# Kernel optimization log

Hardware: AMD Instinct MI355X
Metric: run time of the kernel (lower is better)

Reference implementation:

```python
import jax, jax.numpy as jnp
import numpy as np

N, E, D, ED, H, MAXDEG = 50000, 800000, 128, 64, 8, 512
C = D // H


def _ln(x, g, b, eps=1e-5):
    m = jnp.mean(x, axis=-1, keepdims=True)
    v = jnp.var(x, axis=-1, keepdims=True)
    return (x - m) * jax.lax.rsqrt(v + eps) * g + b


def setup_inputs() -> dict:
    key = jax.random.key(0)
    ks = jax.random.split(key, 16)
    nrm = lambda k, s: jax.random.normal(k, s, jnp.float32) * 0.02
    return {
        "x": jax.random.normal(ks[0], (N, D), jnp.float32),
        "edge_index": jax.random.randint(ks[1], (2, E), 0, N, dtype=jnp.int32),
        "edge_attr": jax.random.normal(ks[2], (E, ED), jnp.float32),
        "deg_emb": nrm(ks[3], (MAXDEG, D)),
        "ln_g": jnp.ones((D,), jnp.float32), "ln_b": jnp.zeros((D,), jnp.float32),
        "Wq": nrm(ks[4], (D, D)), "bq": jnp.zeros((D,), jnp.float32),
        "Wk": nrm(ks[5], (D, D)), "bk": jnp.zeros((D,), jnp.float32),
        "Wv": nrm(ks[6], (D, D)), "bv": jnp.zeros((D,), jnp.float32),
        "We": nrm(ks[7], (ED, D)), "be": jnp.zeros((D,), jnp.float32),
        "Wskip": nrm(ks[8], (D, D)), "bskip": jnp.zeros((D,), jnp.float32),
        "W1": nrm(ks[9], (D, 4 * D)), "b1": jnp.zeros((4 * D,), jnp.float32),
        "W2": nrm(ks[10], (4 * D, D)), "b2": jnp.zeros((D,), jnp.float32),
        "eu_ln_g": jnp.ones((D,), jnp.float32), "eu_ln_b": jnp.zeros((D,), jnp.float32),
        "Wm": nrm(ks[11], (2 * D + ED, 2 * ED)), "bm": jnp.zeros((2 * ED,), jnp.float32),
        "eln_g": jnp.ones((ED,), jnp.float32), "eln_b": jnp.zeros((ED,), jnp.float32),
    }


def reference(x, edge_index, edge_attr, deg_emb, ln_g, ln_b, Wq, bq, Wk, bk, Wv, bv,
              We, be, Wskip, bskip, W1, b1, W2, b2, eu_ln_g, eu_ln_b, Wm, bm, eln_g, eln_b):
    n = x.shape[0]
    src, dst = edge_index[0], edge_index[1]

    # degree embedding: out-degree via scatter-add on src, clamped
    deg = jax.ops.segment_sum(jnp.ones_like(src), src, num_segments=n)
    x_in = x + deg_emb[jnp.clip(deg, 0, MAXDEG - 1)]

    # pre-norm (same LayerNorm module used for attn and ffn branches)
    h = _ln(x_in, ln_g, ln_b)

    # TransformerConv: per-edge gather -> score -> segment softmax -> scatter
    q = (h @ Wq + bq).reshape(n, H, C)
    k = (h @ Wk + bk).reshape(n, H, C)
    v = (h @ Wv + bv).reshape(n, H, C)
    e = (edge_attr @ We + be).reshape(-1, H, C)  # [E,H,C]

    ke = k[src] + e
    alpha = jnp.sum(q[dst] * ke, axis=-1) / jnp.sqrt(jnp.float32(C))  # [E,H]
    amax = jax.ops.segment_max(alpha, dst, num_segments=n)
    amax = jnp.where(jnp.isfinite(amax), amax, 0.0)
    ex = jnp.exp(alpha - amax[dst])
    denom = jax.ops.segment_sum(ex, dst, num_segments=n)
    w = ex / (denom[dst] + 1e-16)  # [E,H]

    msg = (v[src] + e) * w[:, :, None]
    out = jax.ops.segment_sum(msg, dst, num_segments=n).reshape(n, D)
    h_attn = out + h @ Wskip + bskip  # root skip on normed input

    x_attn = x_in + h_attn

    # FFN with pre-norm (norm_type == 'layer')
    hf = _ln(x_attn, ln_g, ln_b)
    ffn = jax.nn.gelu(hf @ W1 + b1, approximate=False) @ W2 + b2
    x_new = x_attn + ffn

    # EdgeUpdate: gated residual MLP on gathered node pairs
    xn = _ln(x_new, eu_ln_g, eu_ln_b)
    m = jnp.concatenate([xn[src], xn[dst], edge_attr], axis=-1)  # [E, 2D+ED]
    raw = jax.nn.relu(m @ Wm + bm)
    delta, gate = jnp.split(raw, 2, axis=-1)
    ea_new = _ln(edge_attr + jax.nn.sigmoid(gate) * delta, eln_g, eln_b)

    return x_new, ea_new
```

## Files before the change

kernel.cpp:

```cpp
#include <hip/hip_runtime.h>
#include <hip/hip_bf16.h>
#include <math.h>

constexpr int N_NODES = 50000;
constexpr int N_EDGES = 800000;
constexpr int D  = 128;
constexpr int ED = 64;

typedef __attribute__((ext_vector_type(8))) short short8;
typedef __attribute__((ext_vector_type(4))) float f32x4;

static __device__ __forceinline__ float allsum64(float v){
#pragma unroll
  for(int off=32; off>=1; off>>=1) v += __shfl_xor(v, off, 64);
  return v;
}

static __device__ __forceinline__ short bfs(float f){
  __hip_bfloat16 h = __float2bfloat16(f);
  return *reinterpret_cast<short*>(&h);
}
static __device__ __forceinline__ float bf2f(short s){
  __hip_bfloat16 h = *reinterpret_cast<__hip_bfloat16*>(&s);
  return __bfloat162float(h);
}

template<typename T> __device__ __forceinline__ T cvt_out(float v);
template<> __device__ __forceinline__ float cvt_out<float>(float v){ return v; }
template<> __device__ __forceinline__ __hip_bfloat16 cvt_out<__hip_bfloat16>(float v){ return __float2bfloat16(v); }

__global__ void k_deg(const int* __restrict__ src, const int* __restrict__ dst,
                      int* __restrict__ deg, int* __restrict__ hist){
  int i = blockIdx.x*256 + threadIdx.x;
  if(i < N_EDGES){
    atomicAdd(&deg[src[i]], 1);
    atomicAdd(&hist[dst[i]], 1);
  }
}

__global__ __launch_bounds__(1024) void k_scan(const int* __restrict__ hist,
                                               int* __restrict__ rows,
                                               int* __restrict__ cursor){
  __shared__ int part[1024];
  const int t = threadIdx.x;
  const int CH = (N_NODES + 1023) / 1024;
  int base = t*CH;
  int s = 0;
  for(int i=0;i<CH;i++){ int idx=base+i; if(idx<N_NODES) s += hist[idx]; }
  part[t] = s; __syncthreads();
  for(int off=1; off<1024; off<<=1){
    int v = (t>=off) ? part[t-off] : 0;
    __syncthreads();
    part[t] += v;
    __syncthreads();
  }
  int run = part[t] - s;
  for(int i=0;i<CH;i++){
    int idx=base+i;
    if(idx<N_NODES){ rows[idx]=run; cursor[idx]=run; run += hist[idx]; }
  }
  if(t==1023) rows[N_NODES] = run;
}

__global__ void k_scatter(const int* __restrict__ src, const int* __restrict__ dst,
                          int* __restrict__ cursor,
                          int* __restrict__ perm, int* __restrict__ ssrc){
  int e = blockIdx.x*256 + threadIdx.x;
  if(e < N_EDGES){
    int p = atomicAdd(&cursor[dst[e]], 1);
    perm[p] = e;
    ssrc[p] = src[e];
  }
}

__global__ __launch_bounds__(256) void k_node_prep(
    const float* __restrict__ x, const int* __restrict__ deg,
    const float* __restrict__ deg_emb, const float* __restrict__ g,
    const float* __restrict__ b, float* __restrict__ xin, float* __restrict__ h){
  int node = blockIdx.x*4 + (threadIdx.x>>6);
  int lane = threadIdx.x & 63;
  if(node >= N_NODES) return;
  int dg = deg[node]; dg = dg > 511 ? 511 : dg;
  const float* xr = x + (size_t)node*D;
  const float* er = deg_emb + (size_t)dg*D;
  float a0 = xr[lane]    + er[lane];
  float a1 = xr[lane+64] + er[lane+64];
  float* xo = xin + (size_t)node*D;
  xo[lane] = a0; xo[lane+64] = a1;
  float s  = allsum64(a0+a1);
  float s2 = allsum64(a0*a0 + a1*a1);
  float mean = s * (1.f/128.f);
  float var  = s2 * (1.f/128.f) - mean*mean;
  float rs = rsqrtf(var + 1e-5f);
  float* ho = h + (size_t)node*D;
  ho[lane]    = (a0-mean)*rs*g[lane]    + b[lane];
  ho[lane+64] = (a1-mean)*rs*g[lane+64] + b[lane+64];
}

__global__ void k_pack(const float* __restrict__ Wq, const float* __restrict__ Wk,
                       const float* __restrict__ Wv, const float* __restrict__ Ws,
                       const float* __restrict__ bq, const float* __restrict__ bk,
                       const float* __restrict__ bv, const float* __restrict__ bs,
                       float* __restrict__ Wcat, float* __restrict__ bcat){
  int idx = blockIdx.x*256 + threadIdx.x;
  if(idx < D*4*D){
    int i = idx >> 9, j = idx & 511;
    int sel = j >> 7, jj = j & 127;
    const float* W = sel==0?Wq: sel==1?Wk: sel==2?Wv:Ws;
    Wcat[idx] = W[i*D + jj];
  } else if(idx < D*4*D + 4*D){
    int j = idx - D*4*D;
    int sel = j>>7, jj = j&127;
    const float* B = sel==0?bq: sel==1?bk: sel==2?bv:bs;
    bcat[j] = B[jj];
  }
}

__global__ void k_packWN(const float* __restrict__ W, short* __restrict__ out,
                         int K, int Nfull){
  int idx = blockIdx.x*256 + threadIdx.x;
  if(idx >= K*Nfull) return;
  int KC = K >> 5;
  int j  = idx & 7;
  int l  = (idx>>3) & 63;
  int cf = (idx>>9) & 7;
  int rest = idx >> 12;
  int kc = rest % KC;
  int nb = rest / KC;
  int k = kc*32 + ((l>>4)<<3) + j;
  int n = nb*128 + (cf<<4) + (l&15);
  out[idx] = bfs(W[(size_t)k*Nfull + n]);
}

template<int ACT, bool SRCADD, typename OutT, typename AT>
__global__ __launch_bounds__(256) void k_gemm_mfma(
    const AT* __restrict__ A, const short* __restrict__ Wp,
    const float* __restrict__ bias, const float* __restrict__ Src,
    OutT* __restrict__ C, int M, int K, int Nfull){
  const int tid = threadIdx.x, lane = tid & 63, wid = tid >> 6;
  const int l16 = lane & 15, lg = lane >> 4;
  const int KC = K >> 5;
  const size_t rowb = (size_t)blockIdx.x*64 + wid*16;
  const int nb = blockIdx.y;
  size_t arow = rowb + l16; if(arow >= (size_t)M) arow = M-1;
  f32x4 acc[8] = {};
  const short8* Bg = ((const short8*)Wp) + (size_t)nb*KC*512 + lane;
  for(int kc=0; kc<KC; kc++){
    short8 a;
    if constexpr (sizeof(AT)==4){
      const float* ap = (const float*)A + arow*K + kc*32 + lg*8;
      float4 f0 = *(const float4*)ap;
      float4 f1 = *(const float4*)(ap+4);
      a[0]=bfs(f0.x); a[1]=bfs(f0.y); a[2]=bfs(f0.z); a[3]=bfs(f0.w);
      a[4]=bfs(f1.x); a[5]=bfs(f1.y); a[6]=bfs(f1.z); a[7]=bfs(f1.w);
    } else {
      a = *(const short8*)((const short*)A + arow*K + kc*32 + lg*8);
    }
#pragma unroll
    for(int cf=0;cf<8;cf++){
      short8 b = Bg[(kc*8+cf)*64];
      acc[cf] = __builtin_amdgcn_mfma_f32_16x16x32_bf16(a, b, acc[cf], 0, 0, 0);
    }
  }
#pragma unroll
  for(int cf=0;cf<8;cf++){
    int col = nb*128 + cf*16 + l16;
    float bb = bias[col];
#pragma unroll
    for(int r=0;r<4;r++){
      size_t ro = rowb + lg*4 + r;
      if(ro < (size_t)M){
        float v = acc[cf][r] + bb;
        if(ACT == 1) v = v * 0.5f * (1.f + erff(v * 0.70710678118f));
        if(SRCADD) v += Src[ro*Nfull + col];
        C[ro*Nfull + col] = cvt_out<OutT>(v);
      }
    }
  }
}

__global__ __launch_bounds__(256) void k_eproj_sorted(
    const float* __restrict__ eattr, const int* __restrict__ perm,
    const short* __restrict__ Wep, const float* __restrict__ be,
    __hip_bfloat16* __restrict__ out){
  const int tid = threadIdx.x, lane = tid & 63, wid = tid >> 6;
  const int l16 = lane & 15, lg = lane >> 4;
  const size_t row = (size_t)blockIdx.x*64 + wid*16;
  const int pe = perm[row + l16];
  f32x4 acc[8] = {};
  const short8* Bg = ((const short8*)Wep) + lane;
  const float* ga = eattr + (size_t)pe*64;
#pragma unroll
  for(int kc=0;kc<2;kc++){
    int cb = kc*32 + lg*8;
    float4 f0 = *(const float4*)(ga + cb);
    float4 f1 = *(const float4*)(ga + cb + 4);
    short8 a;
    a[0]=bfs(f0.x); a[1]=bfs(f0.y); a[2]=bfs(f0.z); a[3]=bfs(f0.w);
    a[4]=bfs(f1.x); a[5]=bfs(f1.y); a[6]=bfs(f1.z); a[7]=bfs(f1.w);
#pragma unroll
    for(int cf=0;cf<8;cf++){
      short8 b = Bg[(kc*8+cf)*64];
      acc[cf] = __builtin_amdgcn_mfma_f32_16x16x32_bf16(a, b, acc[cf], 0, 0, 0);
    }
  }
#pragma unroll
  for(int cf=0;cf<8;cf++){
    int col = cf*16 + l16;
    float bb = be[col];
#pragma unroll
    for(int r=0;r<4;r++){
      size_t ro = row + lg*4 + r;
      out[ro*128 + col] = __float2bfloat16(acc[cf][r] + bb);
    }
  }
}

__global__ __launch_bounds__(256) void k_attn_fused2(
    const int* __restrict__ ssrc, const int* __restrict__ rows,
    const short* __restrict__ qk, const short* __restrict__ es,
    const float* __restrict__ xin, const float* __restrict__ g,
    const float* __restrict__ b,
    float* __restrict__ xattn, float* __restrict__ hf){
  int n = blockIdx.x*4 + (threadIdx.x>>6);
  int lane = threadIdx.x & 63;
  if(n >= N_NODES) return;
  const short* qrow = qk + (size_t)n*512;
  float q0 = bf2f(qrow[lane]), q1 = bf2f(qrow[lane+64]);
  float m0=-INFINITY, m1=-INFINITY;
  float den0=0.f, den1=0.f, acc0=0.f, acc1=0.f;
  int i = rows[n];
  const int i1 = rows[n+1];

  auto body = [&](float eA0, float eA1, float kv0, float kv1, float kv2, float kv3){
    float p0 = q0*(kv0 + eA0);
    float p1 = q1*(kv1 + eA1);
    p0 += __shfl_xor(p0,1,64); p0 += __shfl_xor(p0,2,64);
    p0 += __shfl_xor(p0,4,64); p0 += __shfl_xor(p0,8,64);
    p1 += __shfl_xor(p1,1,64); p1 += __shfl_xor(p1,2,64);
    p1 += __shfl_xor(p1,4,64); p1 += __shfl_xor(p1,8,64);
    float a0 = p0*0.25f, a1 = p1*0.25f;
    float v0 = kv2 + eA0, v1 = kv3 + eA1;
    float mn0 = fmaxf(m0,a0), mn1 = fmaxf(m1,a1);
    float sc0 = __expf(m0-mn0), sc1 = __expf(m1-mn1);
    float ex0 = __expf(a0-mn0), ex1 = __expf(a1-mn1);
    den0 = den0*sc0 + ex0;       den1 = den1*sc1 + ex1;
    acc0 = acc0*sc0 + ex0*v0;    acc1 = acc1*sc1 + ex1*v1;
    m0 = mn0; m1 = mn1;
  };

  for(; i+2 <= i1; i += 2){
    int sA = ssrc[i], sB = ssrc[i+1];
    const short* eA = es + (size_t)i*128;
    const short* kA = qk + (size_t)sA*512 + 128;
    const short* kB = qk + (size_t)sB*512 + 128;
    float eA0=bf2f(eA[lane]),      eA1=bf2f(eA[lane+64]);
    float eB0=bf2f(eA[lane+128]),  eB1=bf2f(eA[lane+192]);
    float kA0=bf2f(kA[lane]),      kA1=bf2f(kA[lane+64]);
    float vA0=bf2f(kA[lane+128]),  vA1=bf2f(kA[lane+192]);
    float kB0=bf2f(kB[lane]),      kB1=bf2f(kB[lane+64]);
    float vB0=bf2f(kB[lane+128]),  vB1=bf2f(kB[lane+192]);
    float pA0 = q0*(kA0+eA0), pA1 = q1*(kA1+eA1);
    float pB0 = q0*(kB0+eB0), pB1 = q1*(kB1+eB1);
#pragma unroll
    for(int off=1; off<16; off<<=1){
      pA0 += __shfl_xor(pA0,off,64); pA1 += __shfl_xor(pA1,off,64);
      pB0 += __shfl_xor(pB0,off,64); pB1 += __shfl_xor(pB1,off,64);
    }
    {
      float a0 = pA0*0.25f, a1 = pA1*0.25f;
      float v0 = vA0+eA0, v1 = vA1+eA1;
      float mn0 = fmaxf(m0,a0), mn1 = fmaxf(m1,a1);
      float sc0 = __expf(m0-mn0), sc1 = __expf(m1-mn1);
      float ex0 = __expf(a0-mn0), ex1 = __expf(a1-mn1);
      den0 = den0*sc0 + ex0;       den1 = den1*sc1 + ex1;
      acc0 = acc0*sc0 + ex0*v0;    acc1 = acc1*sc1 + ex1*v1;
      m0 = mn0; m1 = mn1;
    }
    {
      float a0 = pB0*0.25f, a1 = pB1*0.25f;
      float v0 = vB0+eB0, v1 = vB1+eB1;
      float mn0 = fmaxf(m0,a0), mn1 = fmaxf(m1,a1);
      float sc0 = __expf(m0-mn0), sc1 = __expf(m1-mn1);
      float ex0 = __expf(a0-mn0), ex1 = __expf(a1-mn1);
      den0 = den0*sc0 + ex0;       den1 = den1*sc1 + ex1;
      acc0 = acc0*sc0 + ex0*v0;    acc1 = acc1*sc1 + ex1*v1;
      m0 = mn0; m1 = mn1;
    }
  }
  if(i < i1){
    int sA = ssrc[i];
    const short* eA = es + (size_t)i*128;
    const short* kA = qk + (size_t)sA*512 + 128;
    body(bf2f(eA[lane]), bf2f(eA[lane+64]),
         bf2f(kA[lane]), bf2f(kA[lane+64]),
         bf2f(kA[lane+128]), bf2f(kA[lane+192]));
  }

  float o0 = acc0/(den0+1e-16f);
  float o1 = acc1/(den1+1e-16f);
  size_t base = (size_t)n*128;
  float a0 = xin[base+lane]    + o0 + bf2f(qrow[lane+384]);
  float a1 = xin[base+lane+64] + o1 + bf2f(qrow[lane+448]);
  xattn[base+lane] = a0; xattn[base+lane+64] = a1;
  float s  = allsum64(a0+a1);
  float s2 = allsum64(a0*a0 + a1*a1);
  float mean = s * (1.f/128.f);
  float var  = s2 * (1.f/128.f) - mean*mean;
  float rs = rsqrtf(var + 1e-5f);
  hf[base+lane]    = (a0-mean)*rs*g[lane]    + b[lane];
  hf[base+lane+64] = (a1-mean)*rs*g[lane+64] + b[lane+64];
}

__global__ __launch_bounds__(256) void k_xn(
    const float* __restrict__ xnew, const float* __restrict__ g,
    const float* __restrict__ b, short* __restrict__ xn){
  int node = blockIdx.x*4 + (threadIdx.x>>6);
  int lane = threadIdx.x & 63;
  if(node >= N_NODES) return;
  size_t base = (size_t)node*D;
  float a0 = xnew[base+lane];
  float a1 = xnew[base+lane+64];
  float s  = allsum64(a0+a1);
  float s2 = allsum64(a0*a0 + a1*a1);
  float mean = s * (1.f/128.f);
  float var  = s2 * (1.f/128.f) - mean*mean;
  float rs = rsqrtf(var + 1e-5f);
  xn[base+lane]    = bfs((a0-mean)*rs*g[lane]    + b[lane]);
  xn[base+lane+64] = bfs((a1-mean)*rs*g[lane+64] + b[lane+64]);
}

__global__ __launch_bounds__(256) void k_edge_mfma4(
    const int* __restrict__ src, const int* __restrict__ dst,
    const short* __restrict__ xnb, const float* __restrict__ ea,
    const short* __restrict__ Wmp, const float* __restrict__ bm,
    const float* __restrict__ eg, const float* __restrict__ ebv,
    float* __restrict__ out){
  const int tid = threadIdx.x, lane = tid & 63, wid = tid >> 6;
  const int l16 = lane & 15, lg = lane >> 4;
  const size_t e0 = (size_t)blockIdx.x*128 + wid*32;
  const int ko = lg*8;
  int sI[2], dI[2];
  sI[0] = src[e0+l16];    dI[0] = dst[e0+l16];
  sI[1] = src[e0+16+l16]; dI[1] = dst[e0+16+l16];
  f32x4 acc[8][2] = {};
  const short8* Bg = ((const short8*)Wmp) + lane;

#pragma unroll
  for(int kc=0; kc<10; kc++){
    short8 a[2];
#pragma unroll
    for(int mi=0;mi<2;mi++){
      if(kc < 8){
        int node = (kc < 4) ? sI[mi] : dI[mi];
        a[mi] = *(const short8*)(xnb + (size_t)node*128 + (kc&3)*32 + ko);
      } else {
        const float* ap = ea + (e0 + mi*16 + l16)*64 + (kc-8)*32 + ko;
        float4 f0 = *(const float4*)ap;
        float4 f1 = *(const float4*)(ap+4);
        a[mi][0]=bfs(f0.x); a[mi][1]=bfs(f0.y); a[mi][2]=bfs(f0.z); a[mi][3]=bfs(f0.w);
        a[mi][4]=bfs(f1.x); a[mi][5]=bfs(f1.y); a[mi][6]=bfs(f1.z); a[mi][7]=bfs(f1.w);
      }
    }
#pragma unroll
    for(int cf=0;cf<8;cf++){
      short8 b = Bg[(kc*8+cf)*64];
      acc[cf][0] = __builtin_amdgcn_mfma_f32_16x16x32_bf16(a[0], b, acc[cf][0], 0, 0, 0);
      acc[cf][1] = __builtin_amdgcn_mfma_f32_16x16x32_bf16(a[1], b, acc[cf][1], 0, 0, 0);
    }
  }

  float bmd[4], bmg[4], egc[4], ebc[4];
#pragma unroll
  for(int cf=0;cf<4;cf++){
    int col = cf*16 + l16;
    bmd[cf] = bm[col];
    bmg[cf] = bm[64+col];
    egc[cf] = eg[col];
    ebc[cf] = ebv[col];
  }
#pragma unroll
  for(int mi=0;mi<2;mi++){
#pragma unroll
    for(int r=0;r<4;r++){
      size_t erow = e0 + mi*16 + lg*4 + r;
      float u[4];
      float s1 = 0.f, s2 = 0.f;
#pragma unroll
      for(int cf=0;cf<4;cf++){
        float dlt = fmaxf(0.f, acc[cf][mi][r]   + bmd[cf]);
        float gt  = fmaxf(0.f, acc[cf+4][mi][r] + bmg[cf]);
        float uu = ea[erow*64 + cf*16 + l16] + dlt / (1.f + expf(-gt));
        u[cf] = uu; s1 += uu; s2 += uu*uu;
      }
#pragma unroll
      for(int off=1; off<16; off<<=1){
        s1 += __shfl_xor(s1, off, 64);
        s2 += __shfl_xor(s2, off, 64);
      }
      float mean = s1 * (1.f/64.f);
      float var  = s2 * (1.f/64.f) - mean*mean;
      float rs = rsqrtf(var + 1e-5f);
#pragma unroll
      for(int cf=0;cf<4;cf++)
        out[erow*64 + cf*16 + l16] = (u[cf]-mean)*rs*egc[cf] + ebc[cf];
    }
  }
}

extern "C" void kernel_launch(void* const* d_in, const int* in_sizes, int n_in,
                              void* d_out, int out_size, void* d_ws, size_t ws_size,
                              hipStream_t stream){
  const float* x       = (const float*)d_in[0];
  const int*   eidx    = (const int*)d_in[1];
  const float* eattr   = (const float*)d_in[2];
  const float* deg_emb = (const float*)d_in[3];
  const float* ln_g = (const float*)d_in[4];
  const float* ln_b = (const float*)d_in[5];
  const float* Wq = (const float*)d_in[6];  const float* bq = (const float*)d_in[7];
  const float* Wk = (const float*)d_in[8];  const float* bk = (const float*)d_in[9];
  const float* Wv = (const float*)d_in[10]; const float* bv = (const float*)d_in[11];
  const float* We = (const float*)d_in[12]; const float* be = (const float*)d_in[13];
  const float* Ws = (const float*)d_in[14]; const float* bs = (const float*)d_in[15];
  const float* W1 = (const float*)d_in[16]; const float* b1 = (const float*)d_in[17];
  const float* W2 = (const float*)d_in[18]; const float* b2 = (const float*)d_in[19];
  const float* eug = (const float*)d_in[20]; const float* eub = (const float*)d_in[21];
  const float* Wm = (const float*)d_in[22]; const float* bm = (const float*)d_in[23];
  const float* eg = (const float*)d_in[24]; const float* eb = (const float*)d_in[25];
  (void)in_sizes; (void)n_in; (void)out_size; (void)ws_size;

  const int* src = eidx;
  const int* dst = eidx + N_EDGES;

  float* ws = (float*)d_ws;
  size_t o = 0;
  auto alloc = [&](size_t n){ size_t r = o; o += (n + 63) & ~(size_t)63; return r; };
  size_t o_deg   = alloc(N_NODES);
  size_t o_hist  = alloc(N_NODES);
  size_t zero_f  = o;
  size_t o_rows  = alloc(N_NODES+1);
  size_t o_cur   = alloc(N_NODES);
  size_t o_perm  = alloc(N_EDGES);
  size_t o_ssrc  = alloc(N_EDGES);
  size_t o_attn  = alloc((size_t)N_NODES*D);
  size_t o_xin   = alloc((size_t)N_NODES*D);
  size_t o_h     = alloc((size_t)N_NODES*D);
  size_t o_qkv16 = alloc((size_t)N_NODES*256);
  size_t o_wcat  = alloc((size_t)D*4*D);
  size_t o_bcat  = alloc(4*D);
  size_t o_wqp   = alloc((size_t)128*512/2);
  size_t o_w1p   = alloc((size_t)128*512/2);
  size_t o_w2p   = alloc((size_t)512*128/2);
  size_t o_wmp   = alloc((size_t)320*128/2);
  size_t o_wep   = alloc((size_t)64*128/2);

  float* xnew_out = (float*)d_out;
  float* ea_out   = xnew_out + (size_t)N_NODES*D;
  __hip_bfloat16* es = (__hip_bfloat16*)ea_out;

  hipMemsetAsync(d_ws, 0, zero_f*sizeof(float), stream);

  k_deg<<<(N_EDGES+255)/256, 256, 0, stream>>>(src, dst, (int*)(ws+o_deg),
                                               (int*)(ws+o_hist));
  k_scan<<<1, 1024, 0, stream>>>((int*)(ws+o_hist), (int*)(ws+o_rows),
                                 (int*)(ws+o_cur));
  k_scatter<<<(N_EDGES+255)/256, 256, 0, stream>>>(src, dst, (int*)(ws+o_cur),
                                                   (int*)(ws+o_perm),
                                                   (int*)(ws+o_ssrc));
  k_node_prep<<<N_NODES/4, 256, 0, stream>>>(x, (int*)(ws+o_deg), deg_emb, ln_g, ln_b,
                                             ws+o_xin, ws+o_h);
  k_pack<<<(D*4*D + 4*D + 255)/256, 256, 0, stream>>>(Wq,Wk,Wv,Ws, bq,bk,bv,bs,
                                                      ws+o_wcat, ws+o_bcat);
  k_packWN<<<256, 256, 0, stream>>>(ws+o_wcat, (short*)(ws+o_wqp), 128, 512);
  k_packWN<<<256, 256, 0, stream>>>(W1, (short*)(ws+o_w1p), 128, 512);
  k_packWN<<<256, 256, 0, stream>>>(W2, (short*)(ws+o_w2p), 512, 128);
  k_packWN<<<160, 256, 0, stream>>>(Wm, (short*)(ws+o_wmp), 320, 128);
  k_packWN<<<32,  256, 0, stream>>>(We, (short*)(ws+o_wep), 64, 128);
  {
    dim3 g((N_NODES+63)/64, 4);
    k_gemm_mfma<0,false,__hip_bfloat16,float><<<g,256,0,stream>>>(
        ws+o_h, (const short*)(ws+o_wqp), ws+o_bcat, nullptr,
        (__hip_bfloat16*)(ws+o_qkv16), N_NODES, 128, 512);
  }
  k_eproj_sorted<<<N_EDGES/64, 256, 0, stream>>>(eattr, (const int*)(ws+o_perm),
                                                 (const short*)(ws+o_wep), be, es);
  k_attn_fused2<<<(N_NODES+3)/4, 256, 0, stream>>>((const int*)(ws+o_ssrc),
                                                   (int*)(ws+o_rows),
                                                   (const short*)(ws+o_qkv16),
                                                   (const short*)es,
                                                   ws+o_xin, ln_g, ln_b,
                                                   ws+o_attn, ws+o_h);
  {
    dim3 g((N_NODES+63)/64, 4);
    k_gemm_mfma<1,false,__hip_bfloat16,float><<<g,256,0,stream>>>(
        ws+o_h, (const short*)(ws+o_w1p), b1, nullptr,
        (__hip_bfloat16*)(ws+o_qkv16), N_NODES, 128, 512);
  }
  {
    dim3 g((N_NODES+63)/64, 1);
    k_gemm_mfma<0,true,float,short><<<g,256,0,stream>>>(
        (const short*)(ws+o_qkv16), (const short*)(ws+o_w2p), b2, ws+o_attn,
        xnew_out, N_NODES, 512, 128);
  }
  k_xn<<<N_NODES/4, 256, 0, stream>>>(xnew_out, eug, eub, (short*)(ws+o_xin));
  k_edge_mfma4<<<N_EDGES/128, 256, 0, stream>>>(src, dst, (const short*)(ws+o_xin),
                                                eattr, (const short*)(ws+o_wmp), bm,
                                                eg, eb, ea_out);
}
```

Baseline: 917.3 us.

## Store LN outputs as bf16, interleave QKV/edge layouts, fuse FFN2 with LayerNorm

The pre-norm activations h and hf are now written as bf16 instead of fp32, which halves their traffic and lets the GEMMs read bf16 directly. The QKV GEMM and the edge projection store their outputs with interleaved columns so the attention kernel can fetch q, k/v, e and skip with packed 32/64-bit loads. The FFN second GEMM now adds the residual and computes the edge-update LayerNorm in its epilogue, which removes the separate k_xn pass. The edge MLP kernel prefetches the next A tile into registers before issuing the MFMAs. Rounding to bf16 earlier adds some precision loss, and the permuted layouts have to stay consistent between producer and consumer kernels.

```diff
diff --git a/kernel.cpp b/kernel.cpp
--- a/kernel.cpp
+++ b/kernel.cpp
@@ -24,6 +24,8 @@
   __hip_bfloat16 h = *reinterpret_cast<__hip_bfloat16*>(&s);
   return __bfloat162float(h);
 }
+static __device__ __forceinline__ float lo16(int w){ return bf2f((short)(w & 0xffff)); }
+static __device__ __forceinline__ float hi16(int w){ return bf2f((short)(((unsigned)w) >> 16)); }
 
 template<typename T> __device__ __forceinline__ T cvt_out(float v);
 template<> __device__ __forceinline__ float cvt_out<float>(float v){ return v; }
@@ -76,7 +78,7 @@
 __global__ __launch_bounds__(256) void k_node_prep(
     const float* __restrict__ x, const int* __restrict__ deg,
     const float* __restrict__ deg_emb, const float* __restrict__ g,
-    const float* __restrict__ b, float* __restrict__ xin, float* __restrict__ h){
+    const float* __restrict__ b, float* __restrict__ xin, short* __restrict__ h){
   int node = blockIdx.x*4 + (threadIdx.x>>6);
   int lane = threadIdx.x & 63;
   if(node >= N_NODES) return;
@@ -92,9 +94,8 @@
   float mean = s * (1.f/128.f);
   float var  = s2 * (1.f/128.f) - mean*mean;
   float rs = rsqrtf(var + 1e-5f);
-  float* ho = h + (size_t)node*D;
-  ho[lane]    = (a0-mean)*rs*g[lane]    + b[lane];
-  ho[lane+64] = (a1-mean)*rs*g[lane+64] + b[lane+64];
+  h[(size_t)node*D + lane]    = bfs((a0-mean)*rs*g[lane]    + b[lane]);
+  h[(size_t)node*D + lane+64] = bfs((a1-mean)*rs*g[lane+64] + b[lane+64]);
 }
 
 __global__ void k_pack(const float* __restrict__ Wq, const float* __restrict__ Wk,
@@ -132,10 +133,10 @@
   out[idx] = bfs(W[(size_t)k*Nfull + n]);
 }
 
-template<int ACT, bool SRCADD, typename OutT, typename AT>
+template<int ACT, int OMAP, typename OutT, typename AT>
 __global__ __launch_bounds__(256) void k_gemm_mfma(
     const AT* __restrict__ A, const short* __restrict__ Wp,
-    const float* __restrict__ bias, const float* __restrict__ Src,
+    const float* __restrict__ bias,
     OutT* __restrict__ C, int M, int K, int Nfull){
   const int tid = threadIdx.x, lane = tid & 63, wid = tid >> 6;
   const int l16 = lane & 15, lg = lane >> 4;
@@ -164,16 +165,78 @@
   }
 #pragma unroll
   for(int cf=0;cf<8;cf++){
-    int col = nb*128 + cf*16 + l16;
+    int cIn = cf*16 + l16;
+    int col = nb*128 + cIn;
     float bb = bias[col];
+    int stCol;
+    if(OMAP == 1){
+      if(nb==0)      stCol = 2*(cIn&63) + (cIn>>6);
+      else if(nb==1) stCol = 128 + 4*(cIn&63) + (cIn>>6);
+      else if(nb==2) stCol = 128 + 4*(cIn&63) + 2 + (cIn>>6);
+      else           stCol = 384 + 2*(cIn&63) + (cIn>>6);
+    } else stCol = col;
 #pragma unroll
     for(int r=0;r<4;r++){
       size_t ro = rowb + lg*4 + r;
       if(ro < (size_t)M){
         float v = acc[cf][r] + bb;
         if(ACT == 1) v = v * 0.5f * (1.f + erff(v * 0.70710678118f));
-        if(SRCADD) v += Src[ro*Nfull + col];
-        C[ro*Nfull + col] = cvt_out<OutT>(v);
+        C[ro*Nfull + stCol] = cvt_out<OutT>(v);
+      }
+    }
+  }
+}
+
+__global__ __launch_bounds__(256) void k_ffn2_ln(
+    const short* __restrict__ A, const short* __restrict__ Wp,
+    const float* __restrict__ bias, const float* __restrict__ Src,
+    const float* __restrict__ g, const float* __restrict__ bv,
+    float* __restrict__ xnew, short* __restrict__ xn, int M){
+  const int tid = threadIdx.x, lane = tid & 63, wid = tid >> 6;
+  const int l16 = lane & 15, lg = lane >> 4;
+  const size_t rowb = (size_t)blockIdx.x*64 + wid*16;
+  size_t arow = rowb + l16; if(arow >= (size_t)M) arow = M-1;
+  f32x4 acc[8] = {};
+  const short8* Bg = ((const short8*)Wp) + lane;
+  for(int kc=0; kc<16; kc++){
+    short8 a = *(const short8*)(A + arow*512 + kc*32 + lg*8);
+#pragma unroll
+    for(int cf=0;cf<8;cf++){
+      short8 b = Bg[(kc*8+cf)*64];
+      acc[cf] = __builtin_amdgcn_mfma_f32_16x16x32_bf16(a, b, acc[cf], 0, 0, 0);
+    }
+  }
+  float vals[8][4];
+#pragma unroll
+  for(int cf=0;cf<8;cf++){
+    int col = cf*16 + l16;
+    float bb = bias[col];
+#pragma unroll
+    for(int r=0;r<4;r++){
+      size_t ro = rowb + lg*4 + r; if(ro >= (size_t)M) ro = M-1;
+      vals[cf][r] = acc[cf][r] + bb + Src[ro*128 + col];
+    }
+  }
+#pragma unroll
+  for(int r=0;r<4;r++){
+    float s1 = 0.f, s2 = 0.f;
+#pragma unroll
+    for(int cf=0;cf<8;cf++){ s1 += vals[cf][r]; s2 += vals[cf][r]*vals[cf][r]; }
+#pragma unroll
+    for(int off=1; off<16; off<<=1){
+      s1 += __shfl_xor(s1, off, 64);
+      s2 += __shfl_xor(s2, off, 64);
+    }
+    float mean = s1 * (1.f/128.f);
+    float var  = s2 * (1.f/128.f) - mean*mean;
+    float rs = rsqrtf(var + 1e-5f);
+    size_t ro = rowb + lg*4 + r;
+    if(ro < (size_t)M){
+#pragma unroll
+      for(int cf=0;cf<8;cf++){
+        int col = cf*16 + l16;
+        xnew[ro*128 + col] = vals[cf][r];
+        xn[ro*128 + col] = bfs((vals[cf][r]-mean)*rs*g[col] + bv[col]);
       }
     }
   }
@@ -182,7 +245,7 @@
 __global__ __launch_bounds__(256) void k_eproj_sorted(
     const float* __restrict__ eattr, const int* __restrict__ perm,
     const short* __restrict__ Wep, const float* __restrict__ be,
-    __hip_bfloat16* __restrict__ out){
+    short* __restrict__ out){
   const int tid = threadIdx.x, lane = tid & 63, wid = tid >> 6;
   const int l16 = lane & 15, lg = lane >> 4;
   const size_t row = (size_t)blockIdx.x*64 + wid*16;
@@ -207,130 +270,106 @@
 #pragma unroll
   for(int cf=0;cf<8;cf++){
     int col = cf*16 + l16;
+    int stCol = 2*(col&63) + (col>>6);
     float bb = be[col];
 #pragma unroll
     for(int r=0;r<4;r++){
       size_t ro = row + lg*4 + r;
-      out[ro*128 + col] = __float2bfloat16(acc[cf][r] + bb);
-    }
-  }
-}
-
-__global__ __launch_bounds__(256) void k_attn_fused2(
+      out[ro*128 + stCol] = bfs(acc[cf][r] + bb);
+    }
+  }
+}
+
+__global__ __launch_bounds__(256) void k_attn_fused3(
     const int* __restrict__ ssrc, const int* __restrict__ rows,
     const short* __restrict__ qk, const short* __restrict__ es,
     const float* __restrict__ xin, const float* __restrict__ g,
     const float* __restrict__ b,
-    float* __restrict__ xattn, float* __restrict__ hf){
+    float* __restrict__ xattn, short* __restrict__ hf){
   int n = blockIdx.x*4 + (threadIdx.x>>6);
   int lane = threadIdx.x & 63;
   if(n >= N_NODES) return;
   const short* qrow = qk + (size_t)n*512;
-  float q0 = bf2f(qrow[lane]), q1 = bf2f(qrow[lane+64]);
+  int qw = *(const int*)(qrow + 2*lane);
+  float q0 = lo16(qw), q1 = hi16(qw);
   float m0=-INFINITY, m1=-INFINITY;
   float den0=0.f, den1=0.f, acc0=0.f, acc1=0.f;
   int i = rows[n];
   const int i1 = rows[n+1];
 
-  auto body = [&](float eA0, float eA1, float kv0, float kv1, float kv2, float kv3){
-    float p0 = q0*(kv0 + eA0);
-    float p1 = q1*(kv1 + eA1);
-    p0 += __shfl_xor(p0,1,64); p0 += __shfl_xor(p0,2,64);
-    p0 += __shfl_xor(p0,4,64); p0 += __shfl_xor(p0,8,64);
-    p1 += __shfl_xor(p1,1,64); p1 += __shfl_xor(p1,2,64);
-    p1 += __shfl_xor(p1,4,64); p1 += __shfl_xor(p1,8,64);
-    float a0 = p0*0.25f, a1 = p1*0.25f;
-    float v0 = kv2 + eA0, v1 = kv3 + eA1;
+  for(; i+2 <= i1; i += 2){
+    int sA = ssrc[i], sB = ssrc[i+1];
+    int ewA = *(const int*)(es + (size_t)i*128 + 2*lane);
+    int ewB = *(const int*)(es + (size_t)(i+1)*128 + 2*lane);
+    int2 kvA = *(const int2*)(qk + (size_t)sA*512 + 128 + 4*lane);
+    int2 kvB = *(const int2*)(qk + (size_t)sB*512 + 128 + 4*lane);
+    float eA0=lo16(ewA), eA1=hi16(ewA);
+    float eB0=lo16(ewB), eB1=hi16(ewB);
+    float pA0 = q0*(lo16(kvA.x)+eA0), pA1 = q1*(hi16(kvA.x)+eA1);
+    float pB0 = q0*(lo16(kvB.x)+eB0), pB1 = q1*(hi16(kvB.x)+eB1);
+#pragma unroll
+    for(int off=1; off<16; off<<=1){
+      pA0 += __shfl_xor(pA0,off,64); pA1 += __shfl_xor(pA1,off,64);
+      pB0 += __shfl_xor(pB0,off,64); pB1 += __shfl_xor(pB1,off,64);
+    }
+    {
+      float a0 = pA0*0.25f, a1 = pA1*0.25f;
+      float v0 = lo16(kvA.y)+eA0, v1 = hi16(kvA.y)+eA1;
+      float mn0 = fmaxf(m0,a0), mn1 = fmaxf(m1,a1);
+      float sc0 = __expf(m0-mn0), sc1 = __expf(m1-mn1);
+      float ex0 = __expf(a0-mn0), ex1 = __expf(a1-mn1);
+      den0 = den0*sc0 + ex0;       den1 = den1*sc1 + ex1;
+      acc0 = acc0*sc0 + ex0*v0;    acc1 = acc1*sc1 + ex1*v1;
+      m0 = mn0; m1 = mn1;
+    }
+    {
+      float a0 = pB0*0.25f, a1 = pB1*0.25f;
+      float v0 = lo16(kvB.y)+eB0, v1 = hi16(kvB.y)+eB1;
+      float mn0 = fmaxf(m0,a0), mn1 = fmaxf(m1,a1);
+      float sc0 = __expf(m0-mn0), sc1 = __expf(m1-mn1);
+      float ex0 = __expf(a0-mn0), ex1 = __expf(a1-mn1);
+      den0 = den0*sc0 + ex0;       den1 = den1*sc1 + ex1;
+      acc0 = acc0*sc0 + ex0*v0;    acc1 = acc1*sc1 + ex1*v1;
+      m0 = mn0; m1 = mn1;
+    }
+  }
+  if(i < i1){
+    int sA = ssrc[i];
+    int ewA = *(const int*)(es + (size_t)i*128 + 2*lane);
+    int2 kvA = *(const int2*)(qk + (size_t)sA*512 + 128 + 4*lane);
+    float eA0=lo16(ewA), eA1=hi16(ewA);
+    float pA0 = q0*(lo16(kvA.x)+eA0), pA1 = q1*(hi16(kvA.x)+eA1);
+#pragma unroll
+    for(int off=1; off<16; off<<=1){
+      pA0 += __shfl_xor(pA0,off,64); pA1 += __shfl_xor(pA1,off,64);
+    }
+    float a0 = pA0*0.25f, a1 = pA1*0.25f;
+    float v0 = lo16(kvA.y)+eA0, v1 = hi16(kvA.y)+eA1;
     float mn0 = fmaxf(m0,a0), mn1 = fmaxf(m1,a1);
     float sc0 = __expf(m0-mn0), sc1 = __expf(m1-mn1);
     float ex0 = __expf(a0-mn0), ex1 = __expf(a1-mn1);
     den0 = den0*sc0 + ex0;       den1 = den1*sc1 + ex1;
     acc0 = acc0*sc0 + ex0*v0;    acc1 = acc1*sc1 + ex1*v1;
     m0 = mn0; m1 = mn1;
-  };
-
-  for(; i+2 <= i1; i += 2){
-    int sA = ssrc[i], sB = ssrc[i+1];
-    const short* eA = es + (size_t)i*128;
-    const short* kA = qk + (size_t)sA*512 + 128;
-    const short* kB = qk + (size_t)sB*512 + 128;
-    float eA0=bf2f(eA[lane]),      eA1=bf2f(eA[lane+64]);
-    float eB0=bf2f(eA[lane+128]),  eB1=bf2f(eA[lane+192]);
-    float kA0=bf2f(kA[lane]),      kA1=bf2f(kA[lane+64]);
-    float vA0=bf2f(kA[lane+128]),  vA1=bf2f(kA[lane+192]);
-    float kB0=bf2f(kB[lane]),      kB1=bf2f(kB[lane+64]);
-    float vB0=bf2f(kB[lane+128]),  vB1=bf2f(kB[lane+192]);
-    float pA0 = q0*(kA0+eA0), pA1 = q1*(kA1+eA1);
-    float pB0 = q0*(kB0+eB0), pB1 = q1*(kB1+eB1);
-#pragma unroll
-    for(int off=1; off<16; off<<=1){
-      pA0 += __shfl_xor(pA0,off,64); pA1 += __shfl_xor(pA1,off,64);
-      pB0 += __shfl_xor(pB0,off,64); pB1 += __shfl_xor(pB1,off,64);
-    }
-    {
-      float a0 = pA0*0.25f, a1 = pA1*0.25f;
-      float v0 = vA0+eA0, v1 = vA1+eA1;
-      float mn0 = fmaxf(m0,a0), mn1 = fmaxf(m1,a1);
-      float sc0 = __expf(m0-mn0), sc1 = __expf(m1-mn1);
-      float ex0 = __expf(a0-mn0), ex1 = __expf(a1-mn1);
-      den0 = den0*sc0 + ex0;       den1 = den1*sc1 + ex1;
-      acc0 = acc0*sc0 + ex0*v0;    acc1 = acc1*sc1 + ex1*v1;
-      m0 = mn0; m1 = mn1;
-    }
-    {
-      float a0 = pB0*0.25f, a1 = pB1*0.25f;
-      float v0 = vB0+eB0, v1 = vB1+eB1;
-      float mn0 = fmaxf(m0,a0), mn1 = fmaxf(m1,a1);
-      float sc0 = __expf(m0-mn0), sc1 = __expf(m1-mn1);
-      float ex0 = __expf(a0-mn0), ex1 = __expf(a1-mn1);
-      den0 = den0*sc0 + ex0;       den1 = den1*sc1 + ex1;
-      acc0 = acc0*sc0 + ex0*v0;    acc1 = acc1*sc1 + ex1*v1;
-      m0 = mn0; m1 = mn1;
-    }
-  }
-  if(i < i1){
-    int sA = ssrc[i];
-    const short* eA = es + (size_t)i*128;
-    const short* kA = qk + (size_t)sA*512 + 128;
-    body(bf2f(eA[lane]), bf2f(eA[lane+64]),
-         bf2f(kA[lane]), bf2f(kA[lane+64]),
-         bf2f(kA[lane+128]), bf2f(kA[lane+192]));
   }
 
   float o0 = acc0/(den0+1e-16f);
   float o1 = acc1/(den1+1e-16f);
+  int sw = *(const int*)(qrow + 384 + 2*lane);
   size_t base = (size_t)n*128;
-  float a0 = xin[base+lane]    + o0 + bf2f(qrow[lane+384]);
-  float a1 = xin[base+lane+64] + o1 + bf2f(qrow[lane+448]);
+  float a0 = xin[base+lane]    + o0 + lo16(sw);
+  float a1 = xin[base+lane+64] + o1 + hi16(sw);
   xattn[base+lane] = a0; xattn[base+lane+64] = a1;
   float s  = allsum64(a0+a1);
   float s2 = allsum64(a0*a0 + a1*a1);
   float mean = s * (1.f/128.f);
   float var  = s2 * (1.f/128.f) - mean*mean;
   float rs = rsqrtf(var + 1e-5f);
-  hf[base+lane]    = (a0-mean)*rs*g[lane]    + b[lane];
-  hf[base+lane+64] = (a1-mean)*rs*g[lane+64] + b[lane+64];
-}
-
-__global__ __launch_bounds__(256) void k_xn(
-    const float* __restrict__ xnew, const float* __restrict__ g,
-    const float* __restrict__ b, short* __restrict__ xn){
-  int node = blockIdx.x*4 + (threadIdx.x>>6);
-  int lane = threadIdx.x & 63;
-  if(node >= N_NODES) return;
-  size_t base = (size_t)node*D;
-  float a0 = xnew[base+lane];
-  float a1 = xnew[base+lane+64];
-  float s  = allsum64(a0+a1);
-  float s2 = allsum64(a0*a0 + a1*a1);
-  float mean = s * (1.f/128.f);
-  float var  = s2 * (1.f/128.f) - mean*mean;
-  float rs = rsqrtf(var + 1e-5f);
-  xn[base+lane]    = bfs((a0-mean)*rs*g[lane]    + b[lane]);
-  xn[base+lane+64] = bfs((a1-mean)*rs*g[lane+64] + b[lane+64]);
-}
-
-__global__ __launch_bounds__(256) void k_edge_mfma4(
+  hf[base+lane]    = bfs((a0-mean)*rs*g[lane]    + b[lane]);
+  hf[base+lane+64] = bfs((a1-mean)*rs*g[lane+64] + b[lane+64]);
+}
+
+__global__ __launch_bounds__(256) void k_edge_mfma5(
     const int* __restrict__ src, const int* __restrict__ dst,
     const short* __restrict__ xnb, const float* __restrict__ ea,
     const short* __restrict__ Wmp, const float* __restrict__ bm,
@@ -346,9 +385,7 @@
   f32x4 acc[8][2] = {};
   const short8* Bg = ((const short8*)Wmp) + lane;
 
-#pragma unroll
-  for(int kc=0; kc<10; kc++){
-    short8 a[2];
+  auto load_a = [&](int kc, short8* a){
 #pragma unroll
     for(int mi=0;mi<2;mi++){
       if(kc < 8){
@@ -362,12 +399,20 @@
         a[mi][4]=bfs(f1.x); a[mi][5]=bfs(f1.y); a[mi][6]=bfs(f1.z); a[mi][7]=bfs(f1.w);
       }
     }
+  };
+
+  short8 aC[2], aN[2];
+  load_a(0, aC);
+#pragma unroll
+  for(int kc=0; kc<10; kc++){
+    if(kc < 9) load_a(kc+1, aN);
 #pragma unroll
     for(int cf=0;cf<8;cf++){
       short8 b = Bg[(kc*8+cf)*64];
-      acc[cf][0] = __builtin_amdgcn_mfma_f32_16x16x32_bf16(a[0], b, acc[cf][0], 0, 0, 0);
-      acc[cf][1] = __builtin_amdgcn_mfma_f32_16x16x32_bf16(a[1], b, acc[cf][1], 0, 0, 0);
-    }
+      acc[cf][0] = __builtin_amdgcn_mfma_f32_16x16x32_bf16(aC[0], b, acc[cf][0], 0, 0, 0);
+      acc[cf][1] = __builtin_amdgcn_mfma_f32_16x16x32_bf16(aC[1], b, acc[cf][1], 0, 0, 0);
+    }
+    aC[0] = aN[0]; aC[1] = aN[1];
   }
 
   float bmd[4], bmg[4], egc[4], ebc[4];
@@ -444,7 +489,7 @@
   size_t o_ssrc  = alloc(N_EDGES);
   size_t o_attn  = alloc((size_t)N_NODES*D);
   size_t o_xin   = alloc((size_t)N_NODES*D);
-  size_t o_h     = alloc((size_t)N_NODES*D);
+  size_t o_h     = alloc((size_t)N_NODES*D/2);
   size_t o_qkv16 = alloc((size_t)N_NODES*256);
   size_t o_wcat  = alloc((size_t)D*4*D);
   size_t o_bcat  = alloc(4*D);
@@ -456,7 +501,7 @@
 
   float* xnew_out = (float*)d_out;
   float* ea_out   = xnew_out + (size_t)N_NODES*D;
-  __hip_bfloat16* es = (__hip_bfloat16*)ea_out;
+  short* es = (short*)ea_out;
 
   hipMemsetAsync(d_ws, 0, zero_f*sizeof(float), stream);
 
@@ -468,7 +513,7 @@
                                                    (int*)(ws+o_perm),
                                                    (int*)(ws+o_ssrc));
   k_node_prep<<<N_NODES/4, 256, 0, stream>>>(x, (int*)(ws+o_deg), deg_emb, ln_g, ln_b,
-                                             ws+o_xin, ws+o_h);
+                                             ws+o_xin, (short*)(ws+o_h));
   k_pack<<<(D*4*D + 4*D + 255)/256, 256, 0, stream>>>(Wq,Wk,Wv,Ws, bq,bk,bv,bs,
                                                       ws+o_wcat, ws+o_bcat);
   k_packWN<<<256, 256, 0, stream>>>(ws+o_wcat, (short*)(ws+o_wqp), 128, 512);
@@ -478,32 +523,30 @@
   k_packWN<<<32,  256, 0, stream>>>(We, (short*)(ws+o_wep), 64, 128);
   {
     dim3 g((N_NODES+63)/64, 4);
-    k_gemm_mfma<0,false,__hip_bfloat16,float><<<g,256,0,stream>>>(
-        ws+o_h, (const short*)(ws+o_wqp), ws+o_bcat, nullptr,
+    k_gemm_mfma<0,1,__hip_bfloat16,short><<<g,256,0,stream>>>(
+        (const short*)(ws+o_h), (const short*)(ws+o_wqp), ws+o_bcat,
         (__hip_bfloat16*)(ws+o_qkv16), N_NODES, 128, 512);
   }
   k_eproj_sorted<<<N_EDGES/64, 256, 0, stream>>>(eattr, (const int*)(ws+o_perm),
                                                  (const short*)(ws+o_wep), be, es);
-  k_attn_fused2<<<(N_NODES+3)/4, 256, 0, stream>>>((const int*)(ws+o_ssrc),
+  k_attn_fused3<<<(N_NODES+3)/4, 256, 0, stream>>>((const int*)(ws+o_ssrc),
                                                    (int*)(ws+o_rows),
-                                                   (const short*)(ws+o_qkv16),
-                                                   (const short*)es,
+                                                   (const short*)(ws+o_qkv16), es,
                                                    ws+o_xin, ln_g, ln_b,
-                                                   ws+o_attn, ws+o_h);
+                                                   ws+o_attn, (short*)(ws+o_h));
   {
     dim3 g((N_NODES+63)/64, 4);
-    k_gemm_mfma<1,false,__hip_bfloat16,float><<<g,256,0,stream>>>(
-        ws+o_h, (const short*)(ws+o_w1p), b1, nullptr,
+    k_gemm_mfma<1,0,__hip_bfloat16,short><<<g,256,0,stream>>>(
+        (const short*)(ws+o_h), (const short*)(ws+o_w1p), b1,
         (__hip_bfloat16*)(ws+o_qkv16), N_NODES, 128, 512);
   }
   {
-    dim3 g((N_NODES+63)/64, 1);
-    k_gemm_mfma<0,true,float,short><<<g,256,0,stream>>>(
+    dim3 g((N_NODES+63)/64);
+    k_ffn2_ln<<<g,256,0,stream>>>(
         (const short*)(ws+o_qkv16), (const short*)(ws+o_w2p), b2, ws+o_attn,
-        xnew_out, N_NODES, 512, 128);
-  }
-  k_xn<<<N_NODES/4, 256, 0, stream>>>(xnew_out, eug, eub, (short*)(ws+o_xin));
-  k_edge_mfma4<<<N_EDGES/128, 256, 0, stream>>>(src, dst, (const short*)(ws+o_xin),
+        eug, eub, xnew_out, (short*)(ws+o_xin), N_NODES);
+  }
+  k_edge_mfma5<<<N_EDGES/128, 256, 0, stream>>>(src, dst, (const short*)(ws+o_xin),
                                                 eattr, (const short*)(ws+o_wmp), bm,
                                                 eg, eb, ea_out);
 }
```

After: 948.7 us. +3.4%, slower.
